# Performance work log

Measured on AMD Instinct MI355X. Metric: run time of the kernel, lower is better.

## Reference

```python
import jax, jax.numpy as jnp
import numpy as np

N = 8192          # total points (n_balls * ball_size)
M = 64            # ball_size
NB = N // M       # number of balls
DIM = 64          # feature dim == dimensionality (pe_proj / proj are Identity)
H = 8             # num_heads
EH = DIM // H     # head dim
TOPK = 2          # NSAMSA default topk
MLP = 4           # mlp_ratio
EPS = 1.1920929e-07  # torch RMSNorm default eps = float32 machine eps


def rmsnorm(x, w):
    return x * jax.lax.rsqrt(jnp.mean(x * x, axis=-1, keepdims=True) + EPS) * w


def nsamsa(x, pos):
    # relative position of each leaf wrt its ball center (computed under no_grad in torch)
    pb = jax.lax.stop_gradient(pos).reshape(NB, M, DIM)
    rel = (pb - pb.mean(axis=1, keepdims=True)).reshape(N, DIM)
    x = x + rel  # pe_proj is Identity, so dimensionality == dim

    # tempIdfn + rearrange makes q = k = v = head-split x
    q = x.reshape(N, H, EH).transpose(1, 0, 2)               # (H, N, EH)
    kb = x.reshape(NB, M, H, EH).transpose(2, 0, 1, 3)       # (H, NB, M, EH) per-ball keys/values

    # ball routing: softmax similarity of each query point to ball-mean keys, then top-k
    keys = kb.mean(axis=2)                                   # (H, NB, EH)
    sim = jax.nn.softmax(jnp.einsum('hne,hbe->hnb', q, keys) * (DIM ** -0.5), axis=-1)
    vals, idx = jax.lax.top_k(sim, TOPK)                     # (H, N, TOPK)
    gates = vals + jax.lax.stop_gradient(1.0 - vals)         # straight-through: forward value 1.0

    # gather selected key/value balls per query point (the irregular-access hot spot)
    hidx = jnp.arange(H)[:, None, None]
    kv_sel = kb[hidx, idx]                                   # (H, N, TOPK, M, EH); k == v here

    # attention: gates multiply k (linear), so apply them to the scores instead of copying k
    scores = jnp.einsum('hne,hntme->hntm', q, kv_sel) * gates[..., None] * (EH ** -0.5)
    attn = jax.nn.softmax(scores.reshape(H, N, TOPK * M), axis=-1)
    out = jnp.einsum('hnj,hnje->hne', attn, kv_sel.reshape(H, N, TOPK * M, EH))
    return out.transpose(1, 0, 2).reshape(N, DIM)            # (N, H*EH) head-major


def swiglu(x, w1, b1, w2, b2, w3, b3):
    h = (x @ w2.T + b2) * jax.nn.silu(x @ w1.T + b1)
    return h @ w3.T + b3


def setup_inputs() -> dict:
    key = jax.random.key(0)
    ks = jax.random.split(key, 8)
    s_in = 1.0 / np.sqrt(DIM)
    s_hid = 1.0 / np.sqrt(DIM * MLP)
    return {
        'x': jax.random.normal(ks[0], (N, DIM), dtype=jnp.float32),
        'pos': jax.random.uniform(ks[1], (N, DIM), dtype=jnp.float32),
        'norm1_w': jnp.ones((DIM,), dtype=jnp.float32),
        'norm2_w': jnp.ones((DIM,), dtype=jnp.float32),
        'w1_w': jax.random.normal(ks[2], (DIM * MLP, DIM), dtype=jnp.float32) * s_in,
        'w1_b': jnp.zeros((DIM * MLP,), dtype=jnp.float32),
        'w2_w': jax.random.normal(ks[3], (DIM * MLP, DIM), dtype=jnp.float32) * s_in,
        'w2_b': jnp.zeros((DIM * MLP,), dtype=jnp.float32),
        'w3_w': jax.random.normal(ks[4], (DIM, DIM * MLP), dtype=jnp.float32) * s_hid,
        'w3_b': jnp.zeros((DIM,), dtype=jnp.float32),
    }


def reference(x, pos, norm1_w, norm2_w, w1_w, w1_b, w2_w, w2_b, w3_w, w3_b):
    # BasicLayer with direction=None, depth=1, rotate=False: one ErwinTransformerBlock
    h = x + nsamsa(rmsnorm(x, norm1_w), pos)
    return h + swiglu(rmsnorm(h, norm2_w), w1_w, w1_b, w2_w, w2_b, w3_w, w3_b)
```

## Files before the change

### kernel.cpp

```cpp
#include <hip/hip_runtime.h>
#include <math.h>

#define NPTS 8192
#define NB   128
#define EPS  1.1920929e-07f

__device__ __forceinline__ float rdlane(float v, int l) {
    return __int_as_float(__builtin_amdgcn_readlane(__float_as_int(v), l));
}

__global__ __launch_bounds__(256) void k_prep(
    const float* __restrict__ x, const float* __restrict__ pos,
    const float* __restrict__ n1w,
    const float* __restrict__ w1, const float* __restrict__ w2,
    const float* __restrict__ w3,
    float* __restrict__ A2, float* __restrict__ bmT,
    float* __restrict__ w1T, float* __restrict__ w2T, float* __restrict__ w3T)
{
    int t = threadIdx.x;
    int blk = blockIdx.x;
    if (blk >= NB) {
        int base = (blk - NB) * 1024 + t * 4;
        #pragma unroll
        for (int c = 0; c < 4; ++c) {
            int idx = base + c;
            if (idx < 16384) {
                int e = idx >> 8, k = idx & 255;
                w1T[idx] = w1[k * 64 + e];
            } else if (idx < 32768) {
                int o = idx - 16384; int e = o >> 8, k = o & 255;
                w2T[o] = w2[k * 64 + e];
            } else {
                int o = idx - 32768; int k = o >> 6, d = o & 63;
                w3T[o] = w3[d * 256 + k];
            }
        }
        return;
    }
    __shared__ float xs[64 * 68];
    __shared__ float ps[64 * 68];
    __shared__ float red[256], red2[256];
    __shared__ float pm[64], rs[64], nw[64];

    const float* xb = x + blk * 4096;
    const float* pb = pos + blk * 4096;
    if (t < 64) nw[t] = n1w[t];
    #pragma unroll
    for (int it = 0; it < 4; ++it) {
        int o4 = t + it * 256;
        int row = o4 >> 4, col = (o4 & 15) * 4;
        float4 xv = ((const float4*)xb)[o4];
        float4 pv = ((const float4*)pb)[o4];
        *(float4*)&xs[row * 68 + col] = xv;
        *(float4*)&ps[row * 68 + col] = pv;
    }
    __syncthreads();
    {
        int mg = t >> 6, d = t & 63;
        float s = 0.f;
        #pragma unroll
        for (int p = 0; p < 16; ++p) s += ps[(mg * 16 + p) * 68 + d];
        red[t] = s;
        int m = t >> 2, q = t & 3;
        float ss = 0.f;
        #pragma unroll
        for (int j = 0; j < 16; ++j) { float v = xs[m * 68 + q * 16 + j]; ss += v * v; }
        red2[t] = ss;
    }
    __syncthreads();
    if (t < 64) {
        pm[t] = (red[t] + red[t + 64] + red[t + 128] + red[t + 192]) * (1.0f / 64.0f);
        float s = red2[t * 4] + red2[t * 4 + 1] + red2[t * 4 + 2] + red2[t * 4 + 3];
        rs[t] = 1.0f / sqrtf(s * (1.0f / 64.0f) + EPS);
    }
    __syncthreads();
    {
        int m = t >> 2, q = t & 3;
        float sc = rs[m];
        #pragma unroll
        for (int j = 0; j < 16; ++j) {
            int d = q * 16 + j;
            int a = m * 68 + d;
            xs[a] = xs[a] * sc * nw[d] + (ps[a] - pm[d]);
        }
    }
    __syncthreads();
    {
        int mg = t >> 6, d = t & 63;
        float s = 0.f;
        #pragma unroll
        for (int p = 0; p < 16; ++p) s += xs[(mg * 16 + p) * 68 + d];
        red[t] = s;
        float* a2b = A2 + blk * 4096;
        #pragma unroll
        for (int it = 0; it < 16; ++it) {
            int o = t + it * 256;
            int e = o & 7, m = (o >> 3) & 63, hh = o >> 9;
            a2b[o] = xs[m * 68 + hh * 8 + e];
        }
    }
    __syncthreads();
    if (t < 64) {
        float s = red[t] + red[t + 64] + red[t + 128] + red[t + 192];
        bmT[t * 128 + blk] = s * (1.0f / 64.0f);
    }
}

__global__ __launch_bounds__(256) void k_attn(
    const float* __restrict__ x, const float* __restrict__ A2,
    const float* __restrict__ bmT, float* __restrict__ hws)
{
    int h = blockIdx.x >> 9;
    int i = ((blockIdx.x & 511) << 4) + (threadIdx.x >> 4);
    int lane = threadIdx.x & 15;
    int bi = i >> 6, mi = i & 63;

    const float* qp = A2 + ((bi * 8 + h) * 64 + mi) * 8;
    float q[8];
    #pragma unroll
    for (int e = 0; e < 8; ++e) q[e] = qp[e];

    const float* bmh = bmT + h * 1024;
    float bv0 = -3.4e38f, bv1 = -3.4e38f;
    int ix0 = 0, ix1 = 0;
    #pragma unroll
    for (int j = 0; j < 8; ++j) {
        int b = lane + j * 16;
        float lg = 0.f;
        #pragma unroll
        for (int e = 0; e < 8; ++e) lg = fmaf(q[e], bmh[e * 128 + b], lg);
        if (lg > bv0)      { bv1 = bv0; ix1 = ix0; bv0 = lg; ix0 = b; }
        else if (lg > bv1) { bv1 = lg; ix1 = b; }
    }
    #pragma unroll
    for (int st = 1; st < 16; st <<= 1) {
        float ov0 = __shfl_xor(bv0, st); int oi0 = __shfl_xor(ix0, st);
        float ov1 = __shfl_xor(bv1, st); int oi1 = __shfl_xor(ix1, st);
        bool aw = (bv0 > ov0) || (bv0 == ov0 && ix0 < oi0);
        if (aw) {
            if ((ov0 > bv1) || (ov0 == bv1 && oi0 < ix1)) { bv1 = ov0; ix1 = oi0; }
        } else {
            if ((bv0 > ov1) || (bv0 == ov1 && ix0 < oi1)) { bv1 = bv0; ix1 = ix0; }
            else                                          { bv1 = ov1; ix1 = oi1; }
            bv0 = ov0; ix0 = oi0;
        }
    }

    const float* k0 = A2 + (ix0 * 8 + h) * 512;
    const float* k1 = A2 + (ix1 * 8 + h) * 512;
    const float SC = 0.35355339059327373f;
    float s0[4], s1[4];
    float mx = -3.4e38f;
    #pragma unroll
    for (int jj = 0; jj < 4; ++jj) {
        int m = lane + jj * 16;
        float4 ra = ((const float4*)(k0 + m * 8))[0];
        float4 rb = ((const float4*)(k0 + m * 8))[1];
        float d0 = q[0]*ra.x + q[1]*ra.y + q[2]*ra.z + q[3]*ra.w
                 + q[4]*rb.x + q[5]*rb.y + q[6]*rb.z + q[7]*rb.w;
        s0[jj] = d0 * SC;
        float4 rc = ((const float4*)(k1 + m * 8))[0];
        float4 rd = ((const float4*)(k1 + m * 8))[1];
        float d1 = q[0]*rc.x + q[1]*rc.y + q[2]*rc.z + q[3]*rc.w
                 + q[4]*rd.x + q[5]*rd.y + q[6]*rd.z + q[7]*rd.w;
        s1[jj] = d1 * SC;
        mx = fmaxf(mx, fmaxf(s0[jj], s1[jj]));
    }
    #pragma unroll
    for (int st = 1; st < 16; st <<= 1) mx = fmaxf(mx, __shfl_xor(mx, st));
    float sum = 0.f;
    #pragma unroll
    for (int jj = 0; jj < 4; ++jj) {
        s0[jj] = expf(s0[jj] - mx); sum += s0[jj];
        s1[jj] = expf(s1[jj] - mx); sum += s1[jj];
    }
    #pragma unroll
    for (int st = 1; st < 16; st <<= 1) sum += __shfl_xor(sum, st);
    float inv = 1.0f / sum;

    float acc[8] = {0,0,0,0,0,0,0,0};
    #pragma unroll
    for (int jj = 0; jj < 4; ++jj) {
        int m = lane + jj * 16;
        float4 ra = ((const float4*)(k0 + m * 8))[0];
        float4 rb = ((const float4*)(k0 + m * 8))[1];
        float p = s0[jj] * inv;
        acc[0] += p*ra.x; acc[1] += p*ra.y; acc[2] += p*ra.z; acc[3] += p*ra.w;
        acc[4] += p*rb.x; acc[5] += p*rb.y; acc[6] += p*rb.z; acc[7] += p*rb.w;
        float4 rc = ((const float4*)(k1 + m * 8))[0];
        float4 rd = ((const float4*)(k1 + m * 8))[1];
        float p2 = s1[jj] * inv;
        acc[0] += p2*rc.x; acc[1] += p2*rc.y; acc[2] += p2*rc.z; acc[3] += p2*rc.w;
        acc[4] += p2*rd.x; acc[5] += p2*rd.y; acc[6] += p2*rd.z; acc[7] += p2*rd.w;
    }
    #pragma unroll
    for (int st = 1; st < 16; st <<= 1) {
        #pragma unroll
        for (int e = 0; e < 8; ++e) acc[e] += __shfl_xor(acc[e], st);
    }
    if (lane < 8) {
        float v = acc[0];
        #pragma unroll
        for (int e = 1; e < 8; ++e) if (lane == e) v = acc[e];
        int off = i * 64 + h * 8 + lane;
        hws[off] = x[off] + v;
    }
}

__global__ __launch_bounds__(256) void k_mlp(
    const float* __restrict__ hws, const float* __restrict__ n2w,
    const float* __restrict__ w1T, const float* __restrict__ b1,
    const float* __restrict__ w2T, const float* __restrict__ b2,
    const float* __restrict__ w3T, const float* __restrict__ b3,
    float* __restrict__ out)
{
    int lane = threadIdx.x & 63;
    int wv = blockIdx.x * 4 + (threadIdx.x >> 6);
    int r0 = wv * 8;

    float hreg[8], hn[8];
    float nw = n2w[lane];
    #pragma unroll
    for (int r = 0; r < 8; ++r) hreg[r] = hws[(r0 + r) * 64 + lane];
    #pragma unroll
    for (int r = 0; r < 8; ++r) {
        float s = hreg[r] * hreg[r];
        #pragma unroll
        for (int st = 1; st < 64; st <<= 1) s += __shfl_xor(s, st);
        float sc = 1.0f / sqrtf(s * (1.0f / 64.0f) + EPS);
        hn[r] = hreg[r] * sc * nw;
    }

    float a1[32], a2[32];
    #pragma unroll
    for (int z = 0; z < 32; ++z) { a1[z] = 0.f; a2[z] = 0.f; }
    #pragma unroll 4
    for (int e = 0; e < 64; ++e) {
        float w1v[4], w2v[4];
        #pragma unroll
        for (int u = 0; u < 4; ++u) {
            w1v[u] = w1T[e * 256 + u * 64 + lane];
            w2v[u] = w2T[e * 256 + u * 64 + lane];
        }
        #pragma unroll
        for (int r = 0; r < 8; ++r) {
            float hb = rdlane(hn[r], e);
            #pragma unroll
            for (int u = 0; u < 4; ++u) {
                a1[u * 8 + r] = fmaf(hb, w1v[u], a1[u * 8 + r]);
                a2[u * 8 + r] = fmaf(hb, w2v[u], a2[u * 8 + r]);
            }
        }
    }

    float hid[32];
    #pragma unroll
    for (int u = 0; u < 4; ++u) {
        float bb1 = b1[u * 64 + lane], bb2 = b2[u * 64 + lane];
        #pragma unroll
        for (int r = 0; r < 8; ++r) {
            float z = a1[u * 8 + r] + bb1;
            float g = z / (1.0f + expf(-z));
            hid[u * 8 + r] = (a2[u * 8 + r] + bb2) * g;
        }
    }

    float acc[8] = {0,0,0,0,0,0,0,0};
    #pragma unroll
    for (int u = 0; u < 4; ++u) {
        #pragma unroll 8
        for (int kl = 0; kl < 64; ++kl) {
            float w3v = w3T[(u * 64 + kl) * 64 + lane];
            #pragma unroll
            for (int r = 0; r < 8; ++r)
                acc[r] = fmaf(rdlane(hid[u * 8 + r], kl), w3v, acc[r]);
        }
    }
    float b3v = b3[lane];
    #pragma unroll
    for (int r = 0; r < 8; ++r)
        out[(r0 + r) * 64 + lane] = hreg[r] + acc[r] + b3v;
}

extern "C" void kernel_launch(void* const* d_in, const int* in_sizes, int n_in,
                              void* d_out, int out_size, void* d_ws, size_t ws_size,
                              hipStream_t stream)
{
    const float* x   = (const float*)d_in[0];
    const float* pos = (const float*)d_in[1];
    const float* n1w = (const float*)d_in[2];
    const float* n2w = (const float*)d_in[3];
    const float* w1  = (const float*)d_in[4];
    const float* b1  = (const float*)d_in[5];
    const float* w2  = (const float*)d_in[6];
    const float* b2  = (const float*)d_in[7];
    const float* w3  = (const float*)d_in[8];
    const float* b3  = (const float*)d_in[9];
    float* outp = (float*)d_out;
    float* ws = (float*)d_ws;

    float* A2  = ws;
    float* bmT = ws + 524288;
    float* hws = ws + 532480;
    float* w1T = ws + 1056768;
    float* w2T = ws + 1073152;
    float* w3T = ws + 1089536;

    k_prep<<<dim3(176), dim3(256), 0, stream>>>(x, pos, n1w, w1, w2, w3,
                                                A2, bmT, w1T, w2T, w3T);
    k_attn<<<dim3(4096), dim3(256), 0, stream>>>(x, A2, bmT, hws);
    k_mlp<<<dim3(256), dim3(256), 0, stream>>>(hws, n2w, w1T, b1, w2T, b2,
                                               w3T, b3, outp);
}
```

Baseline: 130.1 us.

## Interleave MLP weights, vectorize routing loads, cache gathered keys, halve rows per wave

Weight prep now interleaves w1/w2 into float2 pairs and packs w3 into pairs so the MLP kernel issues wider loads. The ball-mean table is laid out per ball with 8 contiguous head-dim values, letting the routing dot products use float4 loads. The gathered key/value rows are kept in registers between the score pass and the value pass instead of being loaded twice. The MLP kernel processes 4 rows per wave instead of 8 over twice as many blocks, trading weight reuse per wave for lower register pressure and more waves in flight.

```diff
diff --git a/kernel.cpp b/kernel.cpp
--- a/kernel.cpp
+++ b/kernel.cpp
@@ -14,8 +14,8 @@
     const float* __restrict__ n1w,
     const float* __restrict__ w1, const float* __restrict__ w2,
     const float* __restrict__ w3,
-    float* __restrict__ A2, float* __restrict__ bmT,
-    float* __restrict__ w1T, float* __restrict__ w2T, float* __restrict__ w3T)
+    float* __restrict__ A2, float* __restrict__ bm2,
+    float* __restrict__ w12, float* __restrict__ w3P)
 {
     int t = threadIdx.x;
     int blk = blockIdx.x;
@@ -24,15 +24,13 @@
         #pragma unroll
         for (int c = 0; c < 4; ++c) {
             int idx = base + c;
-            if (idx < 16384) {
-                int e = idx >> 8, k = idx & 255;
-                w1T[idx] = w1[k * 64 + e];
-            } else if (idx < 32768) {
-                int o = idx - 16384; int e = o >> 8, k = o & 255;
-                w2T[o] = w2[k * 64 + e];
+            if (idx < 32768) {
+                int s = idx & 1, l = (idx >> 1) & 63, u = (idx >> 7) & 3, e = idx >> 9;
+                w12[idx] = (s ? w2 : w1)[(u * 64 + l) * 64 + e];
             } else {
-                int o = idx - 32768; int k = o >> 6, d = o & 63;
-                w3T[o] = w3[d * 256 + k];
+                int o = idx - 32768;
+                int s = o & 1, l = (o >> 1) & 63, kp = o >> 7;
+                w3P[o] = w3[l * 256 + kp * 2 + s];
             }
         }
         return;
@@ -102,13 +100,13 @@
     __syncthreads();
     if (t < 64) {
         float s = red[t] + red[t + 64] + red[t + 128] + red[t + 192];
-        bmT[t * 128 + blk] = s * (1.0f / 64.0f);
+        bm2[(t >> 3) * 1024 + blk * 8 + (t & 7)] = s * (1.0f / 64.0f);
     }
 }
 
 __global__ __launch_bounds__(256) void k_attn(
     const float* __restrict__ x, const float* __restrict__ A2,
-    const float* __restrict__ bmT, float* __restrict__ hws)
+    const float* __restrict__ bm2, float* __restrict__ hws)
 {
     int h = blockIdx.x >> 9;
     int i = ((blockIdx.x & 511) << 4) + (threadIdx.x >> 4);
@@ -116,19 +114,19 @@
     int bi = i >> 6, mi = i & 63;
 
     const float* qp = A2 + ((bi * 8 + h) * 64 + mi) * 8;
-    float q[8];
-    #pragma unroll
-    for (int e = 0; e < 8; ++e) q[e] = qp[e];
-
-    const float* bmh = bmT + h * 1024;
+    float4 qa = ((const float4*)qp)[0];
+    float4 qb = ((const float4*)qp)[1];
+
+    const float* bmh = bm2 + h * 1024;
     float bv0 = -3.4e38f, bv1 = -3.4e38f;
     int ix0 = 0, ix1 = 0;
     #pragma unroll
     for (int j = 0; j < 8; ++j) {
         int b = lane + j * 16;
-        float lg = 0.f;
-        #pragma unroll
-        for (int e = 0; e < 8; ++e) lg = fmaf(q[e], bmh[e * 128 + b], lg);
+        float4 f0 = ((const float4*)(bmh + b * 8))[0];
+        float4 f1 = ((const float4*)(bmh + b * 8))[1];
+        float lg = qa.x*f0.x + qa.y*f0.y + qa.z*f0.z + qa.w*f0.w
+                 + qb.x*f1.x + qb.y*f1.y + qb.z*f1.z + qb.w*f1.w;
         if (lg > bv0)      { bv1 = bv0; ix1 = ix0; bv0 = lg; ix0 = b; }
         else if (lg > bv1) { bv1 = lg; ix1 = b; }
     }
@@ -149,20 +147,21 @@
     const float* k0 = A2 + (ix0 * 8 + h) * 512;
     const float* k1 = A2 + (ix1 * 8 + h) * 512;
     const float SC = 0.35355339059327373f;
+    float4 k0a[4], k0b[4], k1a[4], k1b[4];
     float s0[4], s1[4];
     float mx = -3.4e38f;
     #pragma unroll
     for (int jj = 0; jj < 4; ++jj) {
         int m = lane + jj * 16;
-        float4 ra = ((const float4*)(k0 + m * 8))[0];
-        float4 rb = ((const float4*)(k0 + m * 8))[1];
-        float d0 = q[0]*ra.x + q[1]*ra.y + q[2]*ra.z + q[3]*ra.w
-                 + q[4]*rb.x + q[5]*rb.y + q[6]*rb.z + q[7]*rb.w;
+        k0a[jj] = ((const float4*)(k0 + m * 8))[0];
+        k0b[jj] = ((const float4*)(k0 + m * 8))[1];
+        k1a[jj] = ((const float4*)(k1 + m * 8))[0];
+        k1b[jj] = ((const float4*)(k1 + m * 8))[1];
+        float d0 = qa.x*k0a[jj].x + qa.y*k0a[jj].y + qa.z*k0a[jj].z + qa.w*k0a[jj].w
+                 + qb.x*k0b[jj].x + qb.y*k0b[jj].y + qb.z*k0b[jj].z + qb.w*k0b[jj].w;
         s0[jj] = d0 * SC;
-        float4 rc = ((const float4*)(k1 + m * 8))[0];
-        float4 rd = ((const float4*)(k1 + m * 8))[1];
-        float d1 = q[0]*rc.x + q[1]*rc.y + q[2]*rc.z + q[3]*rc.w
-                 + q[4]*rd.x + q[5]*rd.y + q[6]*rd.z + q[7]*rd.w;
+        float d1 = qa.x*k1a[jj].x + qa.y*k1a[jj].y + qa.z*k1a[jj].z + qa.w*k1a[jj].w
+                 + qb.x*k1b[jj].x + qb.y*k1b[jj].y + qb.z*k1b[jj].z + qb.w*k1b[jj].w;
         s1[jj] = d1 * SC;
         mx = fmaxf(mx, fmaxf(s0[jj], s1[jj]));
     }
@@ -181,17 +180,12 @@
     float acc[8] = {0,0,0,0,0,0,0,0};
     #pragma unroll
     for (int jj = 0; jj < 4; ++jj) {
-        int m = lane + jj * 16;
-        float4 ra = ((const float4*)(k0 + m * 8))[0];
-        float4 rb = ((const float4*)(k0 + m * 8))[1];
         float p = s0[jj] * inv;
-        acc[0] += p*ra.x; acc[1] += p*ra.y; acc[2] += p*ra.z; acc[3] += p*ra.w;
-        acc[4] += p*rb.x; acc[5] += p*rb.y; acc[6] += p*rb.z; acc[7] += p*rb.w;
-        float4 rc = ((const float4*)(k1 + m * 8))[0];
-        float4 rd = ((const float4*)(k1 + m * 8))[1];
+        acc[0] += p*k0a[jj].x; acc[1] += p*k0a[jj].y; acc[2] += p*k0a[jj].z; acc[3] += p*k0a[jj].w;
+        acc[4] += p*k0b[jj].x; acc[5] += p*k0b[jj].y; acc[6] += p*k0b[jj].z; acc[7] += p*k0b[jj].w;
         float p2 = s1[jj] * inv;
-        acc[0] += p2*rc.x; acc[1] += p2*rc.y; acc[2] += p2*rc.z; acc[3] += p2*rc.w;
-        acc[4] += p2*rd.x; acc[5] += p2*rd.y; acc[6] += p2*rd.z; acc[7] += p2*rd.w;
+        acc[0] += p2*k1a[jj].x; acc[1] += p2*k1a[jj].y; acc[2] += p2*k1a[jj].z; acc[3] += p2*k1a[jj].w;
+        acc[4] += p2*k1b[jj].x; acc[5] += p2*k1b[jj].y; acc[6] += p2*k1b[jj].z; acc[7] += p2*k1b[jj].w;
     }
     #pragma unroll
     for (int st = 1; st < 16; st <<= 1) {
@@ -209,21 +203,23 @@
 
 __global__ __launch_bounds__(256) void k_mlp(
     const float* __restrict__ hws, const float* __restrict__ n2w,
-    const float* __restrict__ w1T, const float* __restrict__ b1,
-    const float* __restrict__ w2T, const float* __restrict__ b2,
-    const float* __restrict__ w3T, const float* __restrict__ b3,
-    float* __restrict__ out)
+    const float* __restrict__ w12, const float* __restrict__ b1,
+    const float* __restrict__ b2,  const float* __restrict__ w3P,
+    const float* __restrict__ b3,  float* __restrict__ out)
 {
     int lane = threadIdx.x & 63;
     int wv = blockIdx.x * 4 + (threadIdx.x >> 6);
-    int r0 = wv * 8;
-
-    float hreg[8], hn[8];
+    int r0 = wv * 4;
+
+    const float2* w12v = (const float2*)w12;
+    const float2* w3v  = (const float2*)w3P;
+
+    float hreg[4], hn[4];
     float nw = n2w[lane];
     #pragma unroll
-    for (int r = 0; r < 8; ++r) hreg[r] = hws[(r0 + r) * 64 + lane];
-    #pragma unroll
-    for (int r = 0; r < 8; ++r) {
+    for (int r = 0; r < 4; ++r) hreg[r] = hws[(r0 + r) * 64 + lane];
+    #pragma unroll
+    for (int r = 0; r < 4; ++r) {
         float s = hreg[r] * hreg[r];
         #pragma unroll
         for (int st = 1; st < 64; st <<= 1) s += __shfl_xor(s, st);
@@ -231,55 +227,56 @@
         hn[r] = hreg[r] * sc * nw;
     }
 
-    float a1[32], a2[32];
-    #pragma unroll
-    for (int z = 0; z < 32; ++z) { a1[z] = 0.f; a2[z] = 0.f; }
-    #pragma unroll 4
+    float a1[16], a2[16];
+    #pragma unroll
+    for (int z = 0; z < 16; ++z) { a1[z] = 0.f; a2[z] = 0.f; }
+    #pragma unroll 8
     for (int e = 0; e < 64; ++e) {
-        float w1v[4], w2v[4];
-        #pragma unroll
-        for (int u = 0; u < 4; ++u) {
-            w1v[u] = w1T[e * 256 + u * 64 + lane];
-            w2v[u] = w2T[e * 256 + u * 64 + lane];
-        }
-        #pragma unroll
-        for (int r = 0; r < 8; ++r) {
+        float2 wv0 = w12v[e * 256 + lane];
+        float2 wv1 = w12v[e * 256 + 64 + lane];
+        float2 wv2 = w12v[e * 256 + 128 + lane];
+        float2 wv3 = w12v[e * 256 + 192 + lane];
+        #pragma unroll
+        for (int r = 0; r < 4; ++r) {
             float hb = rdlane(hn[r], e);
-            #pragma unroll
-            for (int u = 0; u < 4; ++u) {
-                a1[u * 8 + r] = fmaf(hb, w1v[u], a1[u * 8 + r]);
-                a2[u * 8 + r] = fmaf(hb, w2v[u], a2[u * 8 + r]);
-            }
-        }
-    }
-
-    float hid[32];
+            a1[r]      = fmaf(hb, wv0.x, a1[r]);      a2[r]      = fmaf(hb, wv0.y, a2[r]);
+            a1[4 + r]  = fmaf(hb, wv1.x, a1[4 + r]);  a2[4 + r]  = fmaf(hb, wv1.y, a2[4 + r]);
+            a1[8 + r]  = fmaf(hb, wv2.x, a1[8 + r]);  a2[8 + r]  = fmaf(hb, wv2.y, a2[8 + r]);
+            a1[12 + r] = fmaf(hb, wv3.x, a1[12 + r]); a2[12 + r] = fmaf(hb, wv3.y, a2[12 + r]);
+        }
+    }
+
+    float hid[16];
     #pragma unroll
     for (int u = 0; u < 4; ++u) {
         float bb1 = b1[u * 64 + lane], bb2 = b2[u * 64 + lane];
         #pragma unroll
-        for (int r = 0; r < 8; ++r) {
-            float z = a1[u * 8 + r] + bb1;
+        for (int r = 0; r < 4; ++r) {
+            float z = a1[u * 4 + r] + bb1;
             float g = z / (1.0f + expf(-z));
-            hid[u * 8 + r] = (a2[u * 8 + r] + bb2) * g;
-        }
-    }
-
-    float acc[8] = {0,0,0,0,0,0,0,0};
+            hid[u * 4 + r] = (a2[u * 4 + r] + bb2) * g;
+        }
+    }
+
+    float acc[4] = {0,0,0,0};
     #pragma unroll
     for (int u = 0; u < 4; ++u) {
         #pragma unroll 8
-        for (int kl = 0; kl < 64; ++kl) {
-            float w3v = w3T[(u * 64 + kl) * 64 + lane];
+        for (int kp = 0; kp < 32; ++kp) {
+            float2 w = w3v[(u * 32 + kp) * 64 + lane];
             #pragma unroll
-            for (int r = 0; r < 8; ++r)
-                acc[r] = fmaf(rdlane(hid[u * 8 + r], kl), w3v, acc[r]);
-        }
-    }
-    float b3v = b3[lane];
-    #pragma unroll
-    for (int r = 0; r < 8; ++r)
-        out[(r0 + r) * 64 + lane] = hreg[r] + acc[r] + b3v;
+            for (int r = 0; r < 4; ++r) {
+                float h0 = rdlane(hid[u * 4 + r], kp * 2);
+                float h1 = rdlane(hid[u * 4 + r], kp * 2 + 1);
+                acc[r] = fmaf(h0, w.x, acc[r]);
+                acc[r] = fmaf(h1, w.y, acc[r]);
+            }
+        }
+    }
+    float b3vv = b3[lane];
+    #pragma unroll
+    for (int r = 0; r < 4; ++r)
+        out[(r0 + r) * 64 + lane] = hreg[r] + acc[r] + b3vv;
 }
 
 extern "C" void kernel_launch(void* const* d_in, const int* in_sizes, int n_in,
@@ -300,15 +297,14 @@
     float* ws = (float*)d_ws;
 
     float* A2  = ws;
-    float* bmT = ws + 524288;
+    float* bm2 = ws + 524288;
     float* hws = ws + 532480;
-    float* w1T = ws + 1056768;
-    float* w2T = ws + 1073152;
-    float* w3T = ws + 1089536;
+    float* w12 = ws + 1056768;
+    float* w3P = ws + 1089536;
 
     k_prep<<<dim3(176), dim3(256), 0, stream>>>(x, pos, n1w, w1, w2, w3,
-                                                A2, bmT, w1T, w2T, w3T);
-    k_attn<<<dim3(4096), dim3(256), 0, stream>>>(x, A2, bmT, hws);
-    k_mlp<<<dim3(256), dim3(256), 0, stream>>>(hws, n2w, w1T, b1, w2T, b2,
-                                               w3T, b3, outp);
-}
+                                                A2, bm2, w12, w3P);
+    k_attn<<<dim3(4096), dim3(256), 0, stream>>>(x, A2, bm2, hws);
+    k_mlp<<<dim3(512), dim3(256), 0, stream>>>(hws, n2w, w12, b1, b2,
+                                               w3P, b3, outp);
+}
```

Result: no change. 130.1 us (-0.0%).
